# Kernel tuning notes

Hardware: AMD Instinct MI355X
Metric: run time of the kernel (lower is better)

The kernel has to match this reference:

```python
import jax, jax.numpy as jnp
import numpy as np

N_NODES = 50000
N_EDGES = 800000
D = 96
H2 = 32
OUT = 4


def _glorot(key, shape):
    fan_in, fan_out = shape[0], shape[1]
    lim = (6.0 / (fan_in + fan_out)) ** 0.5
    return jax.random.uniform(key, shape, jnp.float32, -lim, lim)


def setup_inputs() -> dict:
    key = jax.random.key(0)
    ks = jax.random.split(key, 12)
    x = jax.random.normal(ks[0], (N_NODES, D), jnp.float32)
    edge_index = jax.random.randint(ks[1], (2, N_EDGES), 0, N_NODES, jnp.int32)
    return {
        "x": x,
        "edge_index": edge_index,
        "eps1": jnp.float32(0.0),
        "eps2": jnp.float32(0.0),
        "W1a": _glorot(ks[2], (D, D)),  "b1a": jnp.zeros((D,), jnp.float32),
        "W1b": _glorot(ks[3], (D, D)),  "b1b": jnp.zeros((D,), jnp.float32),
        "W2a": _glorot(ks[4], (D, H2)), "b2a": jnp.zeros((H2,), jnp.float32),
        "W2b": _glorot(ks[5], (H2, H2)),"b2b": jnp.zeros((H2,), jnp.float32),
        "Wh": _glorot(ks[6], (H2, OUT)),"bh": jnp.zeros((OUT,), jnp.float32),
    }


def _gin_agg(h, src, dst):
    # sum_{j in N(i)} h_j : gather source features, scatter-add to destination
    return jax.ops.segment_sum(h[src], dst, num_segments=N_NODES)


def reference(x, edge_index, eps1, eps2, W1a, b1a, W1b, b1b, W2a, b2a, W2b, b2b, Wh, bh):
    src, dst = edge_index[0], edge_index[1]

    # GIN layer 1: mlp1((1+eps1)*x + agg(x)), then outer ReLU (dropout is eval-mode identity)
    z = (1.0 + eps1) * x + _gin_agg(x, src, dst)           # [N, D]
    h = jax.nn.relu(z @ W1a + b1a) @ W1b + b1b             # mlp1
    h = jax.nn.relu(h)

    # GIN layer 2: mlp2((1+eps2)*h + agg(h)), then outer ReLU
    z2 = (1.0 + eps2) * h + _gin_agg(h, src, dst)          # [N, D]
    h2 = jax.nn.relu(z2 @ W2a + b2a) @ W2b + b2b           # mlp2 -> [N, 32]
    h2 = jax.nn.relu(h2)

    return h2 @ Wh + bh                                    # [N, 4]
```

## Files before the change

kernel.cpp:

```cpp
#include <hip/hip_runtime.h>

#define NN 50000
#define NE 800000
#define DD 96
#define HH 32
#define OO 4
#define ELLW 64
#define NBUCK 196
#define BCAP 8192

typedef unsigned short ushort_t;
typedef unsigned int uint_t;
typedef __attribute__((ext_vector_type(8))) short short8;
typedef __attribute__((ext_vector_type(4))) float f32x4;

__device__ inline ushort_t f2bf(float f) {
    uint_t b = __float_as_uint(f);
    return (ushort_t)((b + 0x7fffu + ((b >> 16) & 1u)) >> 16);
}

__device__ inline void addbf8(float* a, uint4 u) {
    a[0] += __uint_as_float(u.x << 16);
    a[1] += __uint_as_float(u.x & 0xffff0000u);
    a[2] += __uint_as_float(u.y << 16);
    a[3] += __uint_as_float(u.y & 0xffff0000u);
    a[4] += __uint_as_float(u.z << 16);
    a[5] += __uint_as_float(u.z & 0xffff0000u);
    a[6] += __uint_as_float(u.w << 16);
    a[7] += __uint_as_float(u.w & 0xffff0000u);
}


#define BA_B   196
#define WF_B   7

__global__ void k_pre(const int* __restrict__ edges, int* __restrict__ bcnt,
                      uint_t* __restrict__ packed,
                      const float* __restrict__ W1b, const float* __restrict__ W2a,
                      const float* __restrict__ W2b, const float* __restrict__ Wh,
                      ushort_t* __restrict__ wf) {
    int b = blockIdx.x;
    if (b < BA_B) {
        __shared__ int hist[NBUCK];
        __shared__ int basesh[NBUCK];
        int thr = threadIdx.x;
        if (thr < NBUCK) hist[thr] = 0;
        __syncthreads();
#pragma unroll
        for (int k = 0; k < 4; ++k) {
            int t4 = b * 1024 + k * 256 + thr;
            if (t4 < NE / 4) {
                int4 tt = ((const int4*)(edges + NE))[t4];
                atomicAdd(&hist[tt.x >> 8], 1);
                atomicAdd(&hist[tt.y >> 8], 1);
                atomicAdd(&hist[tt.z >> 8], 1);
                atomicAdd(&hist[tt.w >> 8], 1);
            }
        }
        __syncthreads();
        if (thr < NBUCK) {
            int c = hist[thr];
            basesh[thr] = c ? atomicAdd(&bcnt[thr], c) : 0;
        }
        __syncthreads();
        if (thr < NBUCK) hist[thr] = 0;
        __syncthreads();
#pragma unroll
        for (int k = 0; k < 4; ++k) {
            int t4 = b * 1024 + k * 256 + thr;
            if (t4 < NE / 4) {
                int4 ss = ((const int4*)edges)[t4];
                int4 tt = ((const int4*)(edges + NE))[t4];
                int b0 = tt.x >> 8, b1 = tt.y >> 8, b2 = tt.z >> 8, b3 = tt.w >> 8;
                int p0 = basesh[b0] + atomicAdd(&hist[b0], 1);
                int p1 = basesh[b1] + atomicAdd(&hist[b1], 1);
                int p2 = basesh[b2] + atomicAdd(&hist[b2], 1);
                int p3 = basesh[b3] + atomicAdd(&hist[b3], 1);
                if (p0 < BCAP) packed[(size_t)b0 * BCAP + p0] = ((uint_t)ss.x << 8) | (tt.x & 255);
                if (p1 < BCAP) packed[(size_t)b1 * BCAP + p1] = ((uint_t)ss.y << 8) | (tt.y & 255);
                if (p2 < BCAP) packed[(size_t)b2 * BCAP + p2] = ((uint_t)ss.z << 8) | (tt.z & 255);
                if (p3 < BCAP) packed[(size_t)b3 * BCAP + p3] = ((uint_t)ss.w << 8) | (tt.w & 255);
            }
        }
        return;
    }
    b -= BA_B;
    int tw = b * 256 + threadIdx.x;
    if (tw < 1728) {
        ushort_t v[8];
        ushort_t* dst;
        if (tw < 1152) {
            int fl = tw;
            int lane = fl & 63, fc = fl >> 6;
            int c = fc % 3, nt = fc / 3;
            int kb = c * 32 + (lane >> 4) * 8;
            int col = nt * 16 + (lane & 15);
#pragma unroll
            for (int j = 0; j < 8; ++j) v[j] = f2bf(W1b[(size_t)(kb + j) * DD + col]);
            dst = wf + (size_t)fl * 8;
        } else if (tw < 1536) {
            int fl = tw - 1152;
            int lane = fl & 63, fc = fl >> 6;
            int c = fc % 3, nt = fc / 3;
            int kb = c * 32 + (lane >> 4) * 8;
            int col = nt * 16 + (lane & 15);
#pragma unroll
            for (int j = 0; j < 8; ++j) v[j] = f2bf(W2a[(size_t)(kb + j) * HH + col]);
            dst = wf + 9216 + (size_t)fl * 8;
        } else if (tw < 1664) {
            int fl = tw - 1536;
            int lane = fl & 63, nt = fl >> 6;
            int kb = (lane >> 4) * 8;
            int col = nt * 16 + (lane & 15);
#pragma unroll
            for (int j = 0; j < 8; ++j) v[j] = f2bf(W2b[(size_t)(kb + j) * HH + col]);
            dst = wf + 12288 + (size_t)fl * 8;
        } else {
            int fl = tw - 1664;
            int lane = fl;
            int kb = (lane >> 4) * 8;
            int col = lane & 15;
#pragma unroll
            for (int j = 0; j < 8; ++j)
                v[j] = (col < OO) ? f2bf(Wh[(size_t)(kb + j) * OO + col]) : (ushort_t)0;
            dst = wf + 13312 + (size_t)fl * 8;
        }
        *(uint4*)dst = *(uint4*)v;
    }
}


#define MT1    (NN / 16)
#define MFMA1_B ((MT1 + 3) / 4)

__global__ void k_main(const int* __restrict__ bcnt, const uint_t* __restrict__ packed,
                       ushort_t* __restrict__ ell, int* __restrict__ deg,
                       const float* __restrict__ x, const float* __restrict__ W1a,
                       ushort_t* __restrict__ y1) {
    __shared__ __align__(16) ushort_t lds[1152 * 8];
    int b = blockIdx.x;
    int thr = threadIdx.x;
    if (b < NBUCK) {
        int* curL = (int*)lds;
        int n0 = b * 256;
        curL[thr] = 0;
        __syncthreads();
        int cnt = min(bcnt[b], BCAP);
        const uint_t* pk = packed + (size_t)b * BCAP;
        for (int e = thr; e < cnt; e += 256) {
            uint_t u = pk[e];
            int doff = u & 255;
            int src = u >> 8;
            int p = atomicAdd(&curL[doff], 1);
            if (p < ELLW) ell[(size_t)(n0 + doff) * ELLW + p] = (ushort_t)src;
        }
        __syncthreads();
        if (n0 + thr < NN) deg[n0 + thr] = curL[thr];
        return;
    }
    b -= NBUCK;
    constexpr int KC = 3, NT = 6;
    for (int fl = thr; fl < 1152; fl += 256) {
        int lane_f = fl & 63;
        int fc = fl >> 6;
        int c = fc % 3, nt = fc / 3;
        int kb = c * 32 + (lane_f >> 4) * 8;
        int col = nt * 16 + (lane_f & 15);
        ushort_t v[8];
#pragma unroll
        for (int j = 0; j < 8; ++j)
            v[j] = f2bf(W1a[(size_t)(kb + j) * DD + col]);
        *(uint4*)(lds + (size_t)fl * 8) = *(uint4*)v;
    }
    __syncthreads();

    int lane = thr & 63;
    int widx = thr >> 6;
    int tile = b * 4 + widx;
    if (tile >= MT1) return;
    int row0 = tile * 16;
    int q = lane >> 4;
    int l16 = lane & 15;

    short8 bf[NT][KC];
#pragma unroll
    for (int nt = 0; nt < NT; ++nt)
#pragma unroll
        for (int c = 0; c < KC; ++c)
            bf[nt][c] = *(short8*)(lds + ((size_t)(nt * 3 + c) * 64 + lane) * 8);

    short8 af[KC];
#pragma unroll
    for (int c = 0; c < KC; ++c) {
        const float* ap = x + (size_t)(row0 + l16) * DD + c * 32 + q * 8;
        float4 f0 = *(const float4*)ap;
        float4 f1 = *(const float4*)(ap + 4);
        ushort_t v[8] = {f2bf(f0.x), f2bf(f0.y), f2bf(f0.z), f2bf(f0.w),
                         f2bf(f1.x), f2bf(f1.y), f2bf(f1.z), f2bf(f1.w)};
        af[c] = *(short8*)v;
    }

    f32x4 acc[NT];
#pragma unroll
    for (int nt = 0; nt < NT; ++nt) acc[nt] = (f32x4){0.f, 0.f, 0.f, 0.f};
#pragma unroll
    for (int nt = 0; nt < NT; ++nt)
#pragma unroll
        for (int c = 0; c < KC; ++c)
            acc[nt] = __builtin_amdgcn_mfma_f32_16x16x32_bf16(af[c], bf[nt][c], acc[nt], 0, 0, 0);

#pragma unroll
    for (int nt = 0; nt < NT; ++nt) {
        int s = nt >> 1;
        int c32 = (nt & 1) * 16 + l16;
#pragma unroll
        for (int r = 0; r < 4; ++r)
            y1[(size_t)s * NN * 32 + (size_t)(row0 + q * 4 + r) * 32 + c32] = f2bf(acc[nt][r]);
    }
}


#define HSTRIDE 104

__global__ void k_aggmm(const ushort_t* __restrict__ y1, const int* __restrict__ deg,
                        const ushort_t* __restrict__ ell, const float* __restrict__ eps_p,
                        const float* __restrict__ b1a, const ushort_t* __restrict__ wf,
                        const float* __restrict__ b1b, ushort_t* __restrict__ y2) {
    constexpr int KC = 3, NT1 = 6, NT2 = 2;
    __shared__ __align__(16) ushort_t hT[64 * HSTRIDE];
    __shared__ __align__(16) ushort_t erL[64 * ELLW];
    __shared__ int degL[64];
    int thr = threadIdx.x;
    int i0 = blockIdx.x * 64;

    for (int t = thr; t < 64 * 8; t += 256) {
        int r = t >> 3, c8 = t & 7;
        int ii = i0 + r;
        uint4 val;
        if (ii < NN) val = ((const uint4*)(ell + (size_t)ii * ELLW))[c8];
        else { val.x = 0; val.y = 0; val.z = 0; val.w = 0; }
        *(uint4*)&erL[r * 64 + c8 * 8] = val;
    }
    if (thr < 64) degL[thr] = (i0 + thr < NN) ? min(deg[i0 + thr], ELLW) : 0;
    __syncthreads();

    int g = thr >> 2;
    int u = thr & 3;
    int i = i0 + g;

    if (i < NN) {
        const ushort_t* er = &erL[g * 64];
        int d = degL[g];
        float e = 1.0f + eps_p[0];
        const float4* b4 = (const float4*)b1a;
        ushort_t* dstg = &hT[g * HSTRIDE + u * 8];
#pragma unroll 1
        for (int s = 0; s < 3; ++s) {
            const uint4* ysS = (const uint4*)(y1 + (size_t)s * NN * 32);
            float a0[8] = {0,0,0,0,0,0,0,0}, a1[8] = {0,0,0,0,0,0,0,0};
            float a2[8] = {0,0,0,0,0,0,0,0}, a3[8] = {0,0,0,0,0,0,0,0};
            int p = 0;
            for (; p + 3 < d; p += 4) {
                int s0 = er[p], s1 = er[p + 1], s2 = er[p + 2], s3 = er[p + 3];
                uint4 f0 = ysS[(size_t)s0 * 4 + u];
                uint4 f1 = ysS[(size_t)s1 * 4 + u];
                uint4 f2 = ysS[(size_t)s2 * 4 + u];
                uint4 f3 = ysS[(size_t)s3 * 4 + u];
                addbf8(a0, f0); addbf8(a1, f1); addbf8(a2, f2); addbf8(a3, f3);
            }
            for (; p < d; ++p) addbf8(a0, ysS[(size_t)er[p] * 4 + u]);

            uint4 su = ysS[(size_t)i * 4 + u];
            float s8[8];
            s8[0] = __uint_as_float(su.x << 16); s8[1] = __uint_as_float(su.x & 0xffff0000u);
            s8[2] = __uint_as_float(su.y << 16); s8[3] = __uint_as_float(su.y & 0xffff0000u);
            s8[4] = __uint_as_float(su.z << 16); s8[5] = __uint_as_float(su.z & 0xffff0000u);
            s8[6] = __uint_as_float(su.w << 16); s8[7] = __uint_as_float(su.w & 0xffff0000u);
            float4 bl = b4[s * 8 + u * 2];
            float4 bh2 = b4[s * 8 + u * 2 + 1];
            float bb[8] = {bl.x, bl.y, bl.z, bl.w, bh2.x, bh2.y, bh2.z, bh2.w};
            ushort_t r[8];
#pragma unroll
            for (int k = 0; k < 8; ++k) {
                float vv = fmaf(e, s8[k], (a0[k] + a1[k]) + (a2[k] + a3[k])) + bb[k];
                r[k] = f2bf(fmaxf(vv, 0.0f));
            }
            *(uint4*)(dstg + s * 32) = *(uint4*)r;
        }
    }
    __syncthreads();

    int lane = thr & 63;
    int widx = thr >> 6;
    int tile = blockIdx.x * 4 + widx;
    if (tile >= MT1) return;
    int row0 = tile * 16;
    int q = lane >> 4;
    int l16 = lane & 15;
    const short8* bfp1 = (const short8*)wf;
    const short8* bfp2 = (const short8*)(wf + 9216);

    short8 bf[NT1][KC];
#pragma unroll
    for (int nt = 0; nt < NT1; ++nt)
#pragma unroll
        for (int c = 0; c < KC; ++c)
            bf[nt][c] = bfp1[(nt * KC + c) * 64 + lane];

    short8 af2[KC];
#pragma unroll
    for (int c = 0; c < KC; ++c) {
        uint4 av = *(const uint4*)&hT[(widx * 16 + l16) * HSTRIDE + c * 32 + q * 8];
        af2[c] = *(short8*)&av;
    }

    f32x4 acc[NT1];
#pragma unroll
    for (int nt = 0; nt < NT1; ++nt) acc[nt] = (f32x4){0.f, 0.f, 0.f, 0.f};
#pragma unroll
    for (int nt = 0; nt < NT1; ++nt)
#pragma unroll
        for (int c = 0; c < KC; ++c)
            acc[nt] = __builtin_amdgcn_mfma_f32_16x16x32_bf16(af2[c], bf[nt][c], acc[nt], 0, 0, 0);

    __syncthreads();
#pragma unroll
    for (int nt = 0; nt < NT1; ++nt) {
        int col = nt * 16 + l16;
        float bv = b1b[col];
#pragma unroll
        for (int r = 0; r < 4; ++r)
            hT[(widx * 16 + q * 4 + r) * HSTRIDE + col] = f2bf(fmaxf(acc[nt][r] + bv, 0.0f));
    }
    __syncthreads();

    short8 af3[KC];
#pragma unroll
    for (int c = 0; c < KC; ++c) {
        uint4 av = *(const uint4*)&hT[(widx * 16 + l16) * HSTRIDE + c * 32 + q * 8];
        af3[c] = *(short8*)&av;
    }
    short8 bf2[NT2][KC];
#pragma unroll
    for (int nt = 0; nt < NT2; ++nt)
#pragma unroll
        for (int c = 0; c < KC; ++c)
            bf2[nt][c] = bfp2[(nt * KC + c) * 64 + lane];

    f32x4 acc2[NT2];
#pragma unroll
    for (int nt = 0; nt < NT2; ++nt) acc2[nt] = (f32x4){0.f, 0.f, 0.f, 0.f};
#pragma unroll
    for (int nt = 0; nt < NT2; ++nt)
#pragma unroll
        for (int c = 0; c < KC; ++c)
            acc2[nt] = __builtin_amdgcn_mfma_f32_16x16x32_bf16(af3[c], bf2[nt][c], acc2[nt], 0, 0, 0);

#pragma unroll
    for (int nt = 0; nt < NT2; ++nt) {
        int col = nt * 16 + l16;
#pragma unroll
        for (int r = 0; r < 4; ++r)
            y2[(size_t)(row0 + q * 4 + r) * HH + col] = f2bf(acc2[nt][r]);
    }
}


#define TS2 40

__global__ void k_agg2tail(const ushort_t* __restrict__ y2, const int* __restrict__ deg,
                           const ushort_t* __restrict__ ell, const float* __restrict__ eps_p,
                           const float* __restrict__ b2a, const float* __restrict__ b2b,
                           const float* __restrict__ bhp, const ushort_t* __restrict__ wf,
                           float* __restrict__ out) {
    __shared__ __align__(16) ushort_t erL[64 * ELLW];
    __shared__ int degL[64];
    __shared__ __align__(16) ushort_t t2T[64 * TS2];
    __shared__ __align__(16) ushort_t hB[4][16 * TS2];
    int thr = threadIdx.x;
    int i0 = blockIdx.x * 64;

    for (int t = thr; t < 64 * 8; t += 256) {
        int r = t >> 3, c8 = t & 7;
        int ii = i0 + r;
        uint4 val;
        if (ii < NN) val = ((const uint4*)(ell + (size_t)ii * ELLW))[c8];
        else { val.x = 0; val.y = 0; val.z = 0; val.w = 0; }
        *(uint4*)&erL[r * 64 + c8 * 8] = val;
    }
    if (thr < 64) degL[thr] = (i0 + thr < NN) ? min(deg[i0 + thr], ELLW) : 0;
    __syncthreads();

    int g = thr >> 2;
    int u = thr & 3;
    int i = i0 + g;

    if (i < NN) {
        const ushort_t* er = &erL[g * 64];
        int d = degL[g];
        const uint4* y4 = (const uint4*)y2;
        float a0[8] = {0,0,0,0,0,0,0,0}, a1[8] = {0,0,0,0,0,0,0,0};
        float a2[8] = {0,0,0,0,0,0,0,0}, a3[8] = {0,0,0,0,0,0,0,0};
        int p = 0;
        for (; p + 3 < d; p += 4) {
            int s0 = er[p], s1 = er[p + 1], s2 = er[p + 2], s3 = er[p + 3];
            uint4 f0 = y4[(size_t)s0 * 4 + u];
            uint4 f1 = y4[(size_t)s1 * 4 + u];
            uint4 f2 = y4[(size_t)s2 * 4 + u];
            uint4 f3 = y4[(size_t)s3 * 4 + u];
            addbf8(a0, f0); addbf8(a1, f1); addbf8(a2, f2); addbf8(a3, f3);
        }
        for (; p < d; ++p) addbf8(a0, y4[(size_t)er[p] * 4 + u]);

        uint4 su = y4[(size_t)i * 4 + u];
        float s8[8];
        s8[0] = __uint_as_float(su.x << 16); s8[1] = __uint_as_float(su.x & 0xffff0000u);
        s8[2] = __uint_as_float(su.y << 16); s8[3] = __uint_as_float(su.y & 0xffff0000u);
        s8[4] = __uint_as_float(su.z << 16); s8[5] = __uint_as_float(su.z & 0xffff0000u);
        s8[6] = __uint_as_float(su.w << 16); s8[7] = __uint_as_float(su.w & 0xffff0000u);
        float4 bl = ((const float4*)b2a)[u * 2];
        float4 bh2 = ((const float4*)b2a)[u * 2 + 1];
        float bb[8] = {bl.x, bl.y, bl.z, bl.w, bh2.x, bh2.y, bh2.z, bh2.w};
        float e = 1.0f + eps_p[0];
        ushort_t r[8];
#pragma unroll
        for (int k = 0; k < 8; ++k) {
            float vv = fmaf(e, s8[k], (a0[k] + a1[k]) + (a2[k] + a3[k])) + bb[k];
            r[k] = f2bf(fmaxf(vv, 0.0f));
        }
        *(uint4*)&t2T[g * TS2 + u * 8] = *(uint4*)r;
    }
    __syncthreads();

    int lane = thr & 63;
    int widx = thr >> 6;
    int tile = blockIdx.x * 4 + widx;
    if (tile >= MT1) return;
    int row0 = tile * 16;
    int q = lane >> 4;
    int l16 = lane & 15;

    uint4 av = *(const uint4*)&t2T[(widx * 16 + l16) * TS2 + q * 8];
    short8 afA = *(short8*)&av;
    const short8* bfW2b = (const short8*)(wf + 12288);
    const short8* bfWh  = (const short8*)(wf + 13312);

    f32x4 acc2[2];
#pragma unroll
    for (int nt = 0; nt < 2; ++nt) {
        acc2[nt] = (f32x4){0.f, 0.f, 0.f, 0.f};
        acc2[nt] = __builtin_amdgcn_mfma_f32_16x16x32_bf16(afA, bfW2b[nt * 64 + lane],
                                                           acc2[nt], 0, 0, 0);
    }

#pragma unroll
    for (int nt = 0; nt < 2; ++nt) {
        int col = nt * 16 + l16;
        float bv = b2b[col];
#pragma unroll
        for (int r = 0; r < 4; ++r)
            hB[widx][(q * 4 + r) * TS2 + col] = f2bf(fmaxf(acc2[nt][r] + bv, 0.0f));
    }

    uint4 av2 = *(const uint4*)&hB[widx][l16 * TS2 + q * 8];
    short8 afH = *(short8*)&av2;
    f32x4 acch = (f32x4){0.f, 0.f, 0.f, 0.f};
    acch = __builtin_amdgcn_mfma_f32_16x16x32_bf16(afH, bfWh[lane], acch, 0, 0, 0);

    if (l16 < OO) {
        float bv = bhp[l16];
#pragma unroll
        for (int r = 0; r < 4; ++r)
            out[(size_t)(row0 + q * 4 + r) * OO + l16] = acch[r] + bv;
    }
}


extern "C" void kernel_launch(void* const* d_in, const int* in_sizes, int n_in,
                              void* d_out, int out_size, void* d_ws, size_t ws_size,
                              hipStream_t stream) {
    const float* x    = (const float*)d_in[0];
    const int*   edges= (const int*)d_in[1];
    const float* eps1 = (const float*)d_in[2];
    const float* eps2 = (const float*)d_in[3];
    const float* W1a  = (const float*)d_in[4];
    const float* b1a  = (const float*)d_in[5];
    const float* W1b  = (const float*)d_in[6];
    const float* b1b  = (const float*)d_in[7];
    const float* W2a  = (const float*)d_in[8];
    const float* b2a  = (const float*)d_in[9];
    const float* W2b  = (const float*)d_in[10];
    const float* b2b  = (const float*)d_in[11];
    const float* Wh   = (const float*)d_in[12];
    const float* bh   = (const float*)d_in[13];

    auto al = [](size_t n) { return (n + 255) / 256 * 256; };
    char* w = (char*)d_ws;
    int*      bcnt   = (int*)w;      w += al((size_t)NBUCK * 4);
    uint_t*   packed = (uint_t*)w;   w += al((size_t)NBUCK * BCAP * 4);
    int*      deg    = (int*)w;      w += al((size_t)NN * 4);
    ushort_t* ell    = (ushort_t*)w; w += al((size_t)NN * ELLW * 2);
    ushort_t* wf     = (ushort_t*)w; w += al((size_t)13824 * 2);
    ushort_t* y1     = (ushort_t*)w; w += al((size_t)NN * DD * 2);
    ushort_t* y2     = (ushort_t*)w; w += al((size_t)NN * HH * 2);

    const int B = 256;

    hipMemsetAsync(bcnt, 0, (size_t)NBUCK * 4, stream);
    k_pre<<<BA_B + WF_B, B, 0, stream>>>(edges, bcnt, packed, W1b, W2a, W2b, Wh, wf);
    k_main<<<NBUCK + MFMA1_B, B, 0, stream>>>(bcnt, packed, ell, deg, x, W1a, y1);
    k_aggmm<<<MFMA1_B, B, 0, stream>>>(y1, deg, ell, eps1, b1a, wf, b1b, y2);
    k_agg2tail<<<(NN + 63) / 64, B, 0, stream>>>(y2, deg, ell, eps2, b2a, b2b, bh, wf,
                                                 (float*)d_out);
}
```

Baseline: 153.3 us.

## Move first GEMM into bucketing kernel and split neighbor gathers across thread pairs

The x@W1a MFMA pass moves into the first kernel alongside edge bucketing and weight conversion, and the ELL build becomes its own small kernel, so the dense matmul no longer waits on bucketing. Both aggregation kernels now launch 512 threads per block, with two threads per row/quarter splitting the neighbor list by parity and combining partial sums via shuffle. This doubles memory-level parallelism for the irregular gathers, at the cost of extra shuffles and half the threads idling during the MFMA tail phase.

Measured after the change: 163.1 us. 6.4% more time.

```diff
diff --git a/kernel.cpp b/kernel.cpp
--- a/kernel.cpp
+++ b/kernel.cpp
@@ -33,17 +33,23 @@
 
 #define BA_B   196
 #define WF_B   7
-
-__global__ void k_pre(const int* __restrict__ edges, int* __restrict__ bcnt,
-                      uint_t* __restrict__ packed,
-                      const float* __restrict__ W1b, const float* __restrict__ W2a,
-                      const float* __restrict__ W2b, const float* __restrict__ Wh,
-                      ushort_t* __restrict__ wf) {
+#define MT1    (NN / 16)
+#define MFMA1_B ((MT1 + 3) / 4)
+
+__global__ void k1(const int* __restrict__ edges, int* __restrict__ bcnt,
+                   uint_t* __restrict__ packed,
+                   const float* __restrict__ W1b, const float* __restrict__ W2a,
+                   const float* __restrict__ W2b, const float* __restrict__ Wh,
+                   ushort_t* __restrict__ wf,
+                   const float* __restrict__ x, const float* __restrict__ W1a,
+                   ushort_t* __restrict__ y1) {
+    __shared__ __align__(16) ushort_t lds[1152 * 8];
     int b = blockIdx.x;
+    int thr = threadIdx.x;
+
     if (b < BA_B) {
-        __shared__ int hist[NBUCK];
-        __shared__ int basesh[NBUCK];
-        int thr = threadIdx.x;
+        int* hist = (int*)lds;
+        int* basesh = hist + NBUCK;
         if (thr < NBUCK) hist[thr] = 0;
         __syncthreads();
 #pragma unroll
@@ -85,80 +91,54 @@
         return;
     }
     b -= BA_B;
-    int tw = b * 256 + threadIdx.x;
-    if (tw < 1728) {
-        ushort_t v[8];
-        ushort_t* dst;
-        if (tw < 1152) {
-            int fl = tw;
-            int lane = fl & 63, fc = fl >> 6;
-            int c = fc % 3, nt = fc / 3;
-            int kb = c * 32 + (lane >> 4) * 8;
-            int col = nt * 16 + (lane & 15);
-#pragma unroll
-            for (int j = 0; j < 8; ++j) v[j] = f2bf(W1b[(size_t)(kb + j) * DD + col]);
-            dst = wf + (size_t)fl * 8;
-        } else if (tw < 1536) {
-            int fl = tw - 1152;
-            int lane = fl & 63, fc = fl >> 6;
-            int c = fc % 3, nt = fc / 3;
-            int kb = c * 32 + (lane >> 4) * 8;
-            int col = nt * 16 + (lane & 15);
-#pragma unroll
-            for (int j = 0; j < 8; ++j) v[j] = f2bf(W2a[(size_t)(kb + j) * HH + col]);
-            dst = wf + 9216 + (size_t)fl * 8;
-        } else if (tw < 1664) {
-            int fl = tw - 1536;
-            int lane = fl & 63, nt = fl >> 6;
-            int kb = (lane >> 4) * 8;
-            int col = nt * 16 + (lane & 15);
-#pragma unroll
-            for (int j = 0; j < 8; ++j) v[j] = f2bf(W2b[(size_t)(kb + j) * HH + col]);
-            dst = wf + 12288 + (size_t)fl * 8;
-        } else {
-            int fl = tw - 1664;
-            int lane = fl;
-            int kb = (lane >> 4) * 8;
-            int col = lane & 15;
-#pragma unroll
-            for (int j = 0; j < 8; ++j)
-                v[j] = (col < OO) ? f2bf(Wh[(size_t)(kb + j) * OO + col]) : (ushort_t)0;
-            dst = wf + 13312 + (size_t)fl * 8;
-        }
-        *(uint4*)dst = *(uint4*)v;
-    }
-}
-
-
-#define MT1    (NN / 16)
-#define MFMA1_B ((MT1 + 3) / 4)
-
-__global__ void k_main(const int* __restrict__ bcnt, const uint_t* __restrict__ packed,
-                       ushort_t* __restrict__ ell, int* __restrict__ deg,
-                       const float* __restrict__ x, const float* __restrict__ W1a,
-                       ushort_t* __restrict__ y1) {
-    __shared__ __align__(16) ushort_t lds[1152 * 8];
-    int b = blockIdx.x;
-    int thr = threadIdx.x;
-    if (b < NBUCK) {
-        int* curL = (int*)lds;
-        int n0 = b * 256;
-        curL[thr] = 0;
-        __syncthreads();
-        int cnt = min(bcnt[b], BCAP);
-        const uint_t* pk = packed + (size_t)b * BCAP;
-        for (int e = thr; e < cnt; e += 256) {
-            uint_t u = pk[e];
-            int doff = u & 255;
-            int src = u >> 8;
-            int p = atomicAdd(&curL[doff], 1);
-            if (p < ELLW) ell[(size_t)(n0 + doff) * ELLW + p] = (ushort_t)src;
-        }
-        __syncthreads();
-        if (n0 + thr < NN) deg[n0 + thr] = curL[thr];
+
+    if (b < WF_B) {
+        int tw = b * 256 + thr;
+        if (tw < 1728) {
+            ushort_t v[8];
+            ushort_t* dst;
+            if (tw < 1152) {
+                int fl = tw;
+                int lane = fl & 63, fc = fl >> 6;
+                int c = fc % 3, nt = fc / 3;
+                int kb = c * 32 + (lane >> 4) * 8;
+                int col = nt * 16 + (lane & 15);
+#pragma unroll
+                for (int j = 0; j < 8; ++j) v[j] = f2bf(W1b[(size_t)(kb + j) * DD + col]);
+                dst = wf + (size_t)fl * 8;
+            } else if (tw < 1536) {
+                int fl = tw - 1152;
+                int lane = fl & 63, fc = fl >> 6;
+                int c = fc % 3, nt = fc / 3;
+                int kb = c * 32 + (lane >> 4) * 8;
+                int col = nt * 16 + (lane & 15);
+#pragma unroll
+                for (int j = 0; j < 8; ++j) v[j] = f2bf(W2a[(size_t)(kb + j) * HH + col]);
+                dst = wf + 9216 + (size_t)fl * 8;
+            } else if (tw < 1664) {
+                int fl = tw - 1536;
+                int lane = fl & 63, nt = fl >> 6;
+                int kb = (lane >> 4) * 8;
+                int col = nt * 16 + (lane & 15);
+#pragma unroll
+                for (int j = 0; j < 8; ++j) v[j] = f2bf(W2b[(size_t)(kb + j) * HH + col]);
+                dst = wf + 12288 + (size_t)fl * 8;
+            } else {
+                int fl = tw - 1664;
+                int lane = fl;
+                int kb = (lane >> 4) * 8;
+                int col = lane & 15;
+#pragma unroll
+                for (int j = 0; j < 8; ++j)
+                    v[j] = (col < OO) ? f2bf(Wh[(size_t)(kb + j) * OO + col]) : (ushort_t)0;
+                dst = wf + 13312 + (size_t)fl * 8;
+            }
+            *(uint4*)dst = *(uint4*)v;
+        }
         return;
     }
-    b -= NBUCK;
+    b -= WF_B;
+
     constexpr int KC = 3, NT = 6;
     for (int fl = thr; fl < 1152; fl += 256) {
         int lane_f = fl & 63;
@@ -217,6 +197,28 @@
         for (int r = 0; r < 4; ++r)
             y1[(size_t)s * NN * 32 + (size_t)(row0 + q * 4 + r) * 32 + c32] = f2bf(acc[nt][r]);
     }
+}
+
+
+__global__ void k2(const int* __restrict__ bcnt, const uint_t* __restrict__ packed,
+                   ushort_t* __restrict__ ell, int* __restrict__ deg) {
+    __shared__ int curL[256];
+    int b = blockIdx.x;
+    int thr = threadIdx.x;
+    int n0 = b * 256;
+    curL[thr] = 0;
+    __syncthreads();
+    int cnt = min(bcnt[b], BCAP);
+    const uint_t* pk = packed + (size_t)b * BCAP;
+    for (int e = thr; e < cnt; e += 256) {
+        uint_t u = pk[e];
+        int doff = u & 255;
+        int src = u >> 8;
+        int p = atomicAdd(&curL[doff], 1);
+        if (p < ELLW) ell[(size_t)(n0 + doff) * ELLW + p] = (ushort_t)src;
+    }
+    __syncthreads();
+    if (n0 + thr < NN) deg[n0 + thr] = curL[thr];
 }
 
 
@@ -233,8 +235,8 @@
     int thr = threadIdx.x;
     int i0 = blockIdx.x * 64;
 
-    for (int t = thr; t < 64 * 8; t += 256) {
-        int r = t >> 3, c8 = t & 7;
+    {
+        int r = thr >> 3, c8 = thr & 7;
         int ii = i0 + r;
         uint4 val;
         if (ii < NN) val = ((const uint4*)(ell + (size_t)ii * ELLW))[c8];
@@ -244,8 +246,9 @@
     if (thr < 64) degL[thr] = (i0 + thr < NN) ? min(deg[i0 + thr], ELLW) : 0;
     __syncthreads();
 
-    int g = thr >> 2;
+    int g = thr >> 3;
     int u = thr & 3;
+    int part = (thr >> 2) & 1;
     int i = i0 + g;
 
     if (i < NN) {
@@ -259,39 +262,48 @@
             const uint4* ysS = (const uint4*)(y1 + (size_t)s * NN * 32);
             float a0[8] = {0,0,0,0,0,0,0,0}, a1[8] = {0,0,0,0,0,0,0,0};
             float a2[8] = {0,0,0,0,0,0,0,0}, a3[8] = {0,0,0,0,0,0,0,0};
-            int p = 0;
-            for (; p + 3 < d; p += 4) {
-                int s0 = er[p], s1 = er[p + 1], s2 = er[p + 2], s3 = er[p + 3];
+            int p = part;
+            for (; p + 6 < d; p += 8) {
+                int s0 = er[p], s1 = er[p + 2], s2 = er[p + 4], s3 = er[p + 6];
                 uint4 f0 = ysS[(size_t)s0 * 4 + u];
                 uint4 f1 = ysS[(size_t)s1 * 4 + u];
                 uint4 f2 = ysS[(size_t)s2 * 4 + u];
                 uint4 f3 = ysS[(size_t)s3 * 4 + u];
                 addbf8(a0, f0); addbf8(a1, f1); addbf8(a2, f2); addbf8(a3, f3);
             }
-            for (; p < d; ++p) addbf8(a0, ysS[(size_t)er[p] * 4 + u]);
-
-            uint4 su = ysS[(size_t)i * 4 + u];
-            float s8[8];
-            s8[0] = __uint_as_float(su.x << 16); s8[1] = __uint_as_float(su.x & 0xffff0000u);
-            s8[2] = __uint_as_float(su.y << 16); s8[3] = __uint_as_float(su.y & 0xffff0000u);
-            s8[4] = __uint_as_float(su.z << 16); s8[5] = __uint_as_float(su.z & 0xffff0000u);
-            s8[6] = __uint_as_float(su.w << 16); s8[7] = __uint_as_float(su.w & 0xffff0000u);
-            float4 bl = b4[s * 8 + u * 2];
-            float4 bh2 = b4[s * 8 + u * 2 + 1];
-            float bb[8] = {bl.x, bl.y, bl.z, bl.w, bh2.x, bh2.y, bh2.z, bh2.w};
-            ushort_t r[8];
+            for (; p < d; p += 2) addbf8(a0, ysS[(size_t)er[p] * 4 + u]);
+
+            float sm[8];
 #pragma unroll
             for (int k = 0; k < 8; ++k) {
-                float vv = fmaf(e, s8[k], (a0[k] + a1[k]) + (a2[k] + a3[k])) + bb[k];
-                r[k] = f2bf(fmaxf(vv, 0.0f));
-            }
-            *(uint4*)(dstg + s * 32) = *(uint4*)r;
+                sm[k] = (a0[k] + a1[k]) + (a2[k] + a3[k]);
+                sm[k] += __shfl_xor(sm[k], 4);
+            }
+            if (part == 0) {
+                uint4 su = ysS[(size_t)i * 4 + u];
+                float s8[8];
+                s8[0] = __uint_as_float(su.x << 16); s8[1] = __uint_as_float(su.x & 0xffff0000u);
+                s8[2] = __uint_as_float(su.y << 16); s8[3] = __uint_as_float(su.y & 0xffff0000u);
+                s8[4] = __uint_as_float(su.z << 16); s8[5] = __uint_as_float(su.z & 0xffff0000u);
+                s8[6] = __uint_as_float(su.w << 16); s8[7] = __uint_as_float(su.w & 0xffff0000u);
+                float4 bl = b4[s * 8 + u * 2];
+                float4 bh2 = b4[s * 8 + u * 2 + 1];
+                float bb[8] = {bl.x, bl.y, bl.z, bl.w, bh2.x, bh2.y, bh2.z, bh2.w};
+                ushort_t r[8];
+#pragma unroll
+                for (int k = 0; k < 8; ++k) {
+                    float vv = fmaf(e, s8[k], sm[k]) + bb[k];
+                    r[k] = f2bf(fmaxf(vv, 0.0f));
+                }
+                *(uint4*)(dstg + s * 32) = *(uint4*)r;
+            }
         }
     }
     __syncthreads();
 
     int lane = thr & 63;
     int widx = thr >> 6;
+    if (widx >= 4) return;
     int tile = blockIdx.x * 4 + widx;
     if (tile >= MT1) return;
     int row0 = tile * 16;
@@ -380,8 +392,8 @@
     int thr = threadIdx.x;
     int i0 = blockIdx.x * 64;
 
-    for (int t = thr; t < 64 * 8; t += 256) {
-        int r = t >> 3, c8 = t & 7;
+    {
+        int r = thr >> 3, c8 = thr & 7;
         int ii = i0 + r;
         uint4 val;
         if (ii < NN) val = ((const uint4*)(ell + (size_t)ii * ELLW))[c8];
@@ -391,8 +403,9 @@
     if (thr < 64) degL[thr] = (i0 + thr < NN) ? min(deg[i0 + thr], ELLW) : 0;
     __syncthreads();
 
-    int g = thr >> 2;
+    int g = thr >> 3;
     int u = thr & 3;
+    int part = (thr >> 2) & 1;
     int i = i0 + g;
 
     if (i < NN) {
@@ -401,39 +414,48 @@
         const uint4* y4 = (const uint4*)y2;
         float a0[8] = {0,0,0,0,0,0,0,0}, a1[8] = {0,0,0,0,0,0,0,0};
         float a2[8] = {0,0,0,0,0,0,0,0}, a3[8] = {0,0,0,0,0,0,0,0};
-        int p = 0;
-        for (; p + 3 < d; p += 4) {
-            int s0 = er[p], s1 = er[p + 1], s2 = er[p + 2], s3 = er[p + 3];
+        int p = part;
+        for (; p + 6 < d; p += 8) {
+            int s0 = er[p], s1 = er[p + 2], s2 = er[p + 4], s3 = er[p + 6];
             uint4 f0 = y4[(size_t)s0 * 4 + u];
             uint4 f1 = y4[(size_t)s1 * 4 + u];
             uint4 f2 = y4[(size_t)s2 * 4 + u];
             uint4 f3 = y4[(size_t)s3 * 4 + u];
             addbf8(a0, f0); addbf8(a1, f1); addbf8(a2, f2); addbf8(a3, f3);
         }
-        for (; p < d; ++p) addbf8(a0, y4[(size_t)er[p] * 4 + u]);
-
-        uint4 su = y4[(size_t)i * 4 + u];
-        float s8[8];
-        s8[0] = __uint_as_float(su.x << 16); s8[1] = __uint_as_float(su.x & 0xffff0000u);
-        s8[2] = __uint_as_float(su.y << 16); s8[3] = __uint_as_float(su.y & 0xffff0000u);
-        s8[4] = __uint_as_float(su.z << 16); s8[5] = __uint_as_float(su.z & 0xffff0000u);
-        s8[6] = __uint_as_float(su.w << 16); s8[7] = __uint_as_float(su.w & 0xffff0000u);
-        float4 bl = ((const float4*)b2a)[u * 2];
-        float4 bh2 = ((const float4*)b2a)[u * 2 + 1];
-        float bb[8] = {bl.x, bl.y, bl.z, bl.w, bh2.x, bh2.y, bh2.z, bh2.w};
-        float e = 1.0f + eps_p[0];
-        ushort_t r[8];
+        for (; p < d; p += 2) addbf8(a0, y4[(size_t)er[p] * 4 + u]);
+
+        float sm[8];
 #pragma unroll
         for (int k = 0; k < 8; ++k) {
-            float vv = fmaf(e, s8[k], (a0[k] + a1[k]) + (a2[k] + a3[k])) + bb[k];
-            r[k] = f2bf(fmaxf(vv, 0.0f));
-        }
-        *(uint4*)&t2T[g * TS2 + u * 8] = *(uint4*)r;
+            sm[k] = (a0[k] + a1[k]) + (a2[k] + a3[k]);
+            sm[k] += __shfl_xor(sm[k], 4);
+        }
+        if (part == 0) {
+            uint4 su = y4[(size_t)i * 4 + u];
+            float s8[8];
+            s8[0] = __uint_as_float(su.x << 16); s8[1] = __uint_as_float(su.x & 0xffff0000u);
+            s8[2] = __uint_as_float(su.y << 16); s8[3] = __uint_as_float(su.y & 0xffff0000u);
+            s8[4] = __uint_as_float(su.z << 16); s8[5] = __uint_as_float(su.z & 0xffff0000u);
+            s8[6] = __uint_as_float(su.w << 16); s8[7] = __uint_as_float(su.w & 0xffff0000u);
+            float4 bl = ((const float4*)b2a)[u * 2];
+            float4 bh2 = ((const float4*)b2a)[u * 2 + 1];
+            float bb[8] = {bl.x, bl.y, bl.z, bl.w, bh2.x, bh2.y, bh2.z, bh2.w};
+            float e = 1.0f + eps_p[0];
+            ushort_t r[8];
+#pragma unroll
+            for (int k = 0; k < 8; ++k) {
+                float vv = fmaf(e, s8[k], sm[k]) + bb[k];
+                r[k] = f2bf(fmaxf(vv, 0.0f));
+            }
+            *(uint4*)&t2T[g * TS2 + u * 8] = *(uint4*)r;
+        }
     }
     __syncthreads();
 
     int lane = thr & 63;
     int widx = thr >> 6;
+    if (widx >= 4) return;
     int tile = blockIdx.x * 4 + widx;
     if (tile >= MT1) return;
     int row0 = tile * 16;
@@ -504,12 +526,11 @@
     ushort_t* y1     = (ushort_t*)w; w += al((size_t)NN * DD * 2);
     ushort_t* y2     = (ushort_t*)w; w += al((size_t)NN * HH * 2);
 
-    const int B = 256;
-
     hipMemsetAsync(bcnt, 0, (size_t)NBUCK * 4, stream);
-    k_pre<<<BA_B + WF_B, B, 0, stream>>>(edges, bcnt, packed, W1b, W2a, W2b, Wh, wf);
-    k_main<<<NBUCK + MFMA1_B, B, 0, stream>>>(bcnt, packed, ell, deg, x, W1a, y1);
-    k_aggmm<<<MFMA1_B, B, 0, stream>>>(y1, deg, ell, eps1, b1a, wf, b1b, y2);
-    k_agg2tail<<<(NN + 63) / 64, B, 0, stream>>>(y2, deg, ell, eps2, b2a, b2b, bh, wf,
-                                                 (float*)d_out);
-}
+    k1<<<BA_B + WF_B + MFMA1_B, 256, 0, stream>>>(edges, bcnt, packed, W1b, W2a, W2b, Wh,
+                                                  wf, x, W1a, y1);
+    k2<<<NBUCK, 256, 0, stream>>>(bcnt, packed, ell, deg);
+    k_aggmm<<<MFMA1_B, 512, 0, stream>>>(y1, deg, ell, eps1, b1a, wf, b1b, y2);
+    k_agg2tail<<<MFMA1_B, 512, 0, stream>>>(y2, deg, ell, eps2, b2a, b2b, bh, wf,
+                                            (float*)d_out);
+}
```

## Move dense x@W1a GEMM into first kernel alongside bucketing, split ELL build out

Applied to the files above, without the earlier changes.

The x@W1a MFMA tiles, which depend only on x and W1a, now run in the same launch as the edge bucketing and weight prepacking, instead of alongside the ELL construction. ELL construction becomes its own small kernel with only the bucket-count blocks. The aim is to overlap the bandwidth-heavy dense GEMM with the atomic-heavy bucketing pass and shorten the critical path of the second launch. The first kernel now uses a larger shared-memory footprint for all of its blocks, which may lower occupancy for the bucketing blocks.

After: 153.0 us. Within noise of the previous version (-0.2%).

```diff
diff --git a/kernel.cpp b/kernel.cpp
--- a/kernel.cpp
+++ b/kernel.cpp
@@ -33,17 +33,23 @@
 
 #define BA_B   196
 #define WF_B   7
-
-__global__ void k_pre(const int* __restrict__ edges, int* __restrict__ bcnt,
-                      uint_t* __restrict__ packed,
-                      const float* __restrict__ W1b, const float* __restrict__ W2a,
-                      const float* __restrict__ W2b, const float* __restrict__ Wh,
-                      ushort_t* __restrict__ wf) {
+#define MT1    (NN / 16)
+#define MFMA1_B ((MT1 + 3) / 4)
+
+__global__ void k1(const int* __restrict__ edges, int* __restrict__ bcnt,
+                   uint_t* __restrict__ packed,
+                   const float* __restrict__ W1b, const float* __restrict__ W2a,
+                   const float* __restrict__ W2b, const float* __restrict__ Wh,
+                   ushort_t* __restrict__ wf,
+                   const float* __restrict__ x, const float* __restrict__ W1a,
+                   ushort_t* __restrict__ y1) {
+    __shared__ __align__(16) ushort_t lds[1152 * 8];
     int b = blockIdx.x;
+    int thr = threadIdx.x;
+
     if (b < BA_B) {
-        __shared__ int hist[NBUCK];
-        __shared__ int basesh[NBUCK];
-        int thr = threadIdx.x;
+        int* hist = (int*)lds;
+        int* basesh = hist + NBUCK;
         if (thr < NBUCK) hist[thr] = 0;
         __syncthreads();
 #pragma unroll
@@ -85,80 +91,54 @@
         return;
     }
     b -= BA_B;
-    int tw = b * 256 + threadIdx.x;
-    if (tw < 1728) {
-        ushort_t v[8];
-        ushort_t* dst;
-        if (tw < 1152) {
-            int fl = tw;
-            int lane = fl & 63, fc = fl >> 6;
-            int c = fc % 3, nt = fc / 3;
-            int kb = c * 32 + (lane >> 4) * 8;
-            int col = nt * 16 + (lane & 15);
-#pragma unroll
-            for (int j = 0; j < 8; ++j) v[j] = f2bf(W1b[(size_t)(kb + j) * DD + col]);
-            dst = wf + (size_t)fl * 8;
-        } else if (tw < 1536) {
-            int fl = tw - 1152;
-            int lane = fl & 63, fc = fl >> 6;
-            int c = fc % 3, nt = fc / 3;
-            int kb = c * 32 + (lane >> 4) * 8;
-            int col = nt * 16 + (lane & 15);
-#pragma unroll
-            for (int j = 0; j < 8; ++j) v[j] = f2bf(W2a[(size_t)(kb + j) * HH + col]);
-            dst = wf + 9216 + (size_t)fl * 8;
-        } else if (tw < 1664) {
-            int fl = tw - 1536;
-            int lane = fl & 63, nt = fl >> 6;
-            int kb = (lane >> 4) * 8;
-            int col = nt * 16 + (lane & 15);
-#pragma unroll
-            for (int j = 0; j < 8; ++j) v[j] = f2bf(W2b[(size_t)(kb + j) * HH + col]);
-            dst = wf + 12288 + (size_t)fl * 8;
-        } else {
-            int fl = tw - 1664;
-            int lane = fl;
-            int kb = (lane >> 4) * 8;
-            int col = lane & 15;
-#pragma unroll
-            for (int j = 0; j < 8; ++j)
-                v[j] = (col < OO) ? f2bf(Wh[(size_t)(kb + j) * OO + col]) : (ushort_t)0;
-            dst = wf + 13312 + (size_t)fl * 8;
-        }
-        *(uint4*)dst = *(uint4*)v;
-    }
-}
-
-
-#define MT1    (NN / 16)
-#define MFMA1_B ((MT1 + 3) / 4)
-
-__global__ void k_main(const int* __restrict__ bcnt, const uint_t* __restrict__ packed,
-                       ushort_t* __restrict__ ell, int* __restrict__ deg,
-                       const float* __restrict__ x, const float* __restrict__ W1a,
-                       ushort_t* __restrict__ y1) {
-    __shared__ __align__(16) ushort_t lds[1152 * 8];
-    int b = blockIdx.x;
-    int thr = threadIdx.x;
-    if (b < NBUCK) {
-        int* curL = (int*)lds;
-        int n0 = b * 256;
-        curL[thr] = 0;
-        __syncthreads();
-        int cnt = min(bcnt[b], BCAP);
-        const uint_t* pk = packed + (size_t)b * BCAP;
-        for (int e = thr; e < cnt; e += 256) {
-            uint_t u = pk[e];
-            int doff = u & 255;
-            int src = u >> 8;
-            int p = atomicAdd(&curL[doff], 1);
-            if (p < ELLW) ell[(size_t)(n0 + doff) * ELLW + p] = (ushort_t)src;
-        }
-        __syncthreads();
-        if (n0 + thr < NN) deg[n0 + thr] = curL[thr];
+
+    if (b < WF_B) {
+        int tw = b * 256 + thr;
+        if (tw < 1728) {
+            ushort_t v[8];
+            ushort_t* dst;
+            if (tw < 1152) {
+                int fl = tw;
+                int lane = fl & 63, fc = fl >> 6;
+                int c = fc % 3, nt = fc / 3;
+                int kb = c * 32 + (lane >> 4) * 8;
+                int col = nt * 16 + (lane & 15);
+#pragma unroll
+                for (int j = 0; j < 8; ++j) v[j] = f2bf(W1b[(size_t)(kb + j) * DD + col]);
+                dst = wf + (size_t)fl * 8;
+            } else if (tw < 1536) {
+                int fl = tw - 1152;
+                int lane = fl & 63, fc = fl >> 6;
+                int c = fc % 3, nt = fc / 3;
+                int kb = c * 32 + (lane >> 4) * 8;
+                int col = nt * 16 + (lane & 15);
+#pragma unroll
+                for (int j = 0; j < 8; ++j) v[j] = f2bf(W2a[(size_t)(kb + j) * HH + col]);
+                dst = wf + 9216 + (size_t)fl * 8;
+            } else if (tw < 1664) {
+                int fl = tw - 1536;
+                int lane = fl & 63, nt = fl >> 6;
+                int kb = (lane >> 4) * 8;
+                int col = nt * 16 + (lane & 15);
+#pragma unroll
+                for (int j = 0; j < 8; ++j) v[j] = f2bf(W2b[(size_t)(kb + j) * HH + col]);
+                dst = wf + 12288 + (size_t)fl * 8;
+            } else {
+                int fl = tw - 1664;
+                int lane = fl;
+                int kb = (lane >> 4) * 8;
+                int col = lane & 15;
+#pragma unroll
+                for (int j = 0; j < 8; ++j)
+                    v[j] = (col < OO) ? f2bf(Wh[(size_t)(kb + j) * OO + col]) : (ushort_t)0;
+                dst = wf + 13312 + (size_t)fl * 8;
+            }
+            *(uint4*)dst = *(uint4*)v;
+        }
         return;
     }
-    b -= NBUCK;
+    b -= WF_B;
+
     constexpr int KC = 3, NT = 6;
     for (int fl = thr; fl < 1152; fl += 256) {
         int lane_f = fl & 63;
@@ -217,6 +197,28 @@
         for (int r = 0; r < 4; ++r)
             y1[(size_t)s * NN * 32 + (size_t)(row0 + q * 4 + r) * 32 + c32] = f2bf(acc[nt][r]);
     }
+}
+
+
+__global__ void k2(const int* __restrict__ bcnt, const uint_t* __restrict__ packed,
+                   ushort_t* __restrict__ ell, int* __restrict__ deg) {
+    __shared__ int curL[256];
+    int b = blockIdx.x;
+    int thr = threadIdx.x;
+    int n0 = b * 256;
+    curL[thr] = 0;
+    __syncthreads();
+    int cnt = min(bcnt[b], BCAP);
+    const uint_t* pk = packed + (size_t)b * BCAP;
+    for (int e = thr; e < cnt; e += 256) {
+        uint_t u = pk[e];
+        int doff = u & 255;
+        int src = u >> 8;
+        int p = atomicAdd(&curL[doff], 1);
+        if (p < ELLW) ell[(size_t)(n0 + doff) * ELLW + p] = (ushort_t)src;
+    }
+    __syncthreads();
+    if (n0 + thr < NN) deg[n0 + thr] = curL[thr];
 }
 
 
@@ -504,12 +506,11 @@
     ushort_t* y1     = (ushort_t*)w; w += al((size_t)NN * DD * 2);
     ushort_t* y2     = (ushort_t*)w; w += al((size_t)NN * HH * 2);
 
-    const int B = 256;
-
     hipMemsetAsync(bcnt, 0, (size_t)NBUCK * 4, stream);
-    k_pre<<<BA_B + WF_B, B, 0, stream>>>(edges, bcnt, packed, W1b, W2a, W2b, Wh, wf);
-    k_main<<<NBUCK + MFMA1_B, B, 0, stream>>>(bcnt, packed, ell, deg, x, W1a, y1);
-    k_aggmm<<<MFMA1_B, B, 0, stream>>>(y1, deg, ell, eps1, b1a, wf, b1b, y2);
-    k_agg2tail<<<(NN + 63) / 64, B, 0, stream>>>(y2, deg, ell, eps2, b2a, b2b, bh, wf,
-                                                 (float*)d_out);
-}
+    k1<<<BA_B + WF_B + MFMA1_B, 256, 0, stream>>>(edges, bcnt, packed, W1b, W2a, W2b, Wh,
+                                                  wf, x, W1a, y1);
+    k2<<<NBUCK, 256, 0, stream>>>(bcnt, packed, ell, deg);
+    k_aggmm<<<MFMA1_B, 256, 0, stream>>>(y1, deg, ell, eps1, b1a, wf, b1b, y2);
+    k_agg2tail<<<(NN + 63) / 64, 256, 0, stream>>>(y2, deg, ell, eps2, b2a, b2b, bh, wf,
+                                                   (float*)d_out);
+}
```
